# Kernel optimization log

Hardware: AMD Instinct MI355X
Metric: run time of the kernel (lower is better)

The kernel has to match this reference:

```python
import jax, jax.numpy as jnp
import numpy as np

H = 16
D_MODEL = 1024
D_K = D_MODEL // H
WINDOW = 50
ROPE_BASE = 10000.0


def _rope_tables(seq_len, dim, dtype):
    inv_freq = 1.0 / (ROPE_BASE ** (jnp.arange(0, dim, 2, dtype=jnp.float32) / dim))
    t = jnp.arange(seq_len, dtype=jnp.float32)
    freqs = t[:, None] * inv_freq[None, :]          # [S, dim/2]
    emb = jnp.concatenate([freqs, freqs], axis=-1)  # [S, dim]
    return jnp.cos(emb).astype(dtype), jnp.sin(emb).astype(dtype)


def _rotate_half(x):
    d = x.shape[-1] // 2
    return jnp.concatenate([-x[..., d:], x[..., :d]], axis=-1)


def setup_inputs() -> dict:
    key = jax.random.key(0)
    ks = jax.random.split(key, 11)
    B, S = 2, 2048
    scale = 1.0 / np.sqrt(D_MODEL)
    inp = {
        'query': jax.random.normal(ks[0], (B, S, D_MODEL), jnp.float32),
        'key':   jax.random.normal(ks[1], (B, S, D_MODEL), jnp.float32),
        'value': jax.random.normal(ks[2], (B, S, D_MODEL), jnp.float32),
        'Wq': jax.random.normal(ks[3], (D_MODEL, D_MODEL), jnp.float32) * scale,
        'bq': jnp.zeros((D_MODEL,), jnp.float32),
        'Wk': jax.random.normal(ks[4], (D_MODEL, D_MODEL), jnp.float32) * scale,
        'bk': jnp.zeros((D_MODEL,), jnp.float32),
        'Wv': jax.random.normal(ks[5], (D_MODEL, D_MODEL), jnp.float32) * scale,
        'bv': jnp.zeros((D_MODEL,), jnp.float32),
        'Wo': jax.random.normal(ks[6], (D_MODEL, D_MODEL), jnp.float32) * scale,
        'bo': jnp.zeros((D_MODEL,), jnp.float32),
    }
    return inp


def reference(query, key, value, Wq, bq, Wk, bk, Wv, bv, Wo, bo):
    B, S, _ = query.shape
    # QKV projections (torch Linear: x @ W.T + b), split into heads -> [B,H,S,Dk]
    def proj(x, W, b):
        return (x @ W.T + b).reshape(B, S, H, D_K).transpose(0, 2, 1, 3)
    q = proj(query, Wq, bq)
    k = proj(key, Wk, bk)
    v = proj(value, Wv, bv)

    cos, sin = _rope_tables(S, D_K, q.dtype)  # [S, Dk]
    q = q * cos + _rotate_half(q) * sin
    k = k * cos + _rotate_half(k) * sin

    scores = jnp.einsum('bhqd,bhkd->bhqk', q, k) / np.sqrt(D_K)
    # sliding-window mask: |i-j| <= WINDOW
    idx = jnp.arange(S)
    dist = jnp.abs(idx[None, :] - idx[:, None])  # [S, S]
    scores = jnp.where(dist <= WINDOW, scores, jnp.asarray(-1e9, scores.dtype))

    p = jax.nn.softmax(scores, axis=-1)
    out = jnp.einsum('bhqk,bhkd->bhqd', p, v)          # [B,H,S,Dk]
    out = out.transpose(0, 2, 1, 3).reshape(B, S, D_MODEL)
    return out @ Wo.T + bo
```

## Files before the change

kernel.cpp:

```cpp
#include <hip/hip_runtime.h>
#include <hip/hip_bf16.h>
#include <math.h>

typedef __bf16 bf16_t;
typedef __bf16 bf16x8 __attribute__((ext_vector_type(8)));
typedef float floatx4 __attribute__((ext_vector_type(4)));
typedef unsigned int u32;

#define NHEAD 16

__device__ __forceinline__ void gload_lds16(const void* g, void* l) {
    __builtin_amdgcn_global_load_lds((const __attribute__((address_space(1))) u32*)g,
                                     (__attribute__((address_space(3))) u32*)l, 16, 0, 0);
}

__global__ __launch_bounds__(256) void k_prep(
    const float* __restrict__ q, const float* __restrict__ k, const float* __restrict__ v,
    const float* __restrict__ wq, const float* __restrict__ wk,
    const float* __restrict__ wv, const float* __restrict__ wo,
    bf16_t* __restrict__ Xq, bf16_t* __restrict__ Xk, bf16_t* __restrict__ Xv,
    bf16_t* __restrict__ Wqb, bf16_t* __restrict__ Wkb, bf16_t* __restrict__ Wvb,
    bf16_t* __restrict__ Wob, float* __restrict__ ct, float* __restrict__ st)
{
    int b = blockIdx.x;
    if (b < 8192) {
        const float* src; bf16_t* dst; int off;
        if      (b < 2048) { src = q;  dst = Xq;  off = b; }
        else if (b < 4096) { src = k;  dst = Xk;  off = b - 2048; }
        else if (b < 6144) { src = v;  dst = Xv;  off = b - 4096; }
        else if (b < 6656) { src = wq; dst = Wqb; off = b - 6144; }
        else if (b < 7168) { src = wk; dst = Wkb; off = b - 6656; }
        else if (b < 7680) { src = wv; dst = Wvb; off = b - 7168; }
        else               { src = wo; dst = Wob; off = b - 7680; }
        int i = (off * 256 + threadIdx.x) * 8;
        float4 a = *(const float4*)(src + i);
        float4 c = *(const float4*)(src + i + 4);
        bf16x8 o;
        o[0]=(bf16_t)a.x; o[1]=(bf16_t)a.y; o[2]=(bf16_t)a.z; o[3]=(bf16_t)a.w;
        o[4]=(bf16_t)c.x; o[5]=(bf16_t)c.y; o[6]=(bf16_t)c.z; o[7]=(bf16_t)c.w;
        *(bf16x8*)(dst + i) = o;
    } else {
        int idx = (b - 8192) * 256 + threadIdx.x;
        int s = idx >> 5, i = idx & 31;
        float e = (float)(2 * i) / 64.0f;
        float invf = 1.0f / powf(10000.0f, e);
        float ang = (float)s * invf;
        ct[idx] = cosf(ang);
        st[idx] = sinf(ang);
    }
}

__global__ __launch_bounds__(256,2) void k_gemm_qkv(
    const bf16_t* __restrict__ Xq, const bf16_t* __restrict__ Xk, const bf16_t* __restrict__ Xv,
    const bf16_t* __restrict__ Wqb, const bf16_t* __restrict__ Wkb, const bf16_t* __restrict__ Wvb,
    const float* __restrict__ bq, const float* __restrict__ bk, const float* __restrict__ bv,
    bf16_t* __restrict__ Qr, bf16_t* __restrict__ Kr, bf16_t* __restrict__ Vh,
    const float* __restrict__ ct, const float* __restrict__ st)
{
    __shared__ bf16_t As[2][128*32];
    __shared__ bf16_t Bs[2][128*32];

    int b0 = blockIdx.x;
    int wg = (b0 & 7) * 96 + (b0 >> 3);
    int id  = wg >> 8;
    int bid = wg & 255;

    const bf16_t* A   = (id==0) ? Xq  : (id==1) ? Xk  : Xv;
    const bf16_t* Wt  = (id==0) ? Wqb : (id==1) ? Wkb : Wvb;
    const float*  bias= (id==0) ? bq  : (id==1) ? bk  : bv;
    bf16_t* out = (id==0) ? Qr : (id==1) ? Kr : Vh;
    bool do_rope = (id < 2);

    int bm = (bid >> 3) << 7;
    int bn = (bid & 7) << 7;
    int tid = threadIdx.x;
    int l = tid & 63, wid = tid >> 6;
    int wr = wid >> 1, wc = wid & 1;
    int lane16 = l & 15, hi8 = (l >> 4) << 3;

    floatx4 acc[4][4];
    #pragma unroll
    for (int i = 0; i < 4; ++i)
        #pragma unroll
        for (int j = 0; j < 4; ++j) acc[i][j] = (floatx4){0.f,0.f,0.f,0.f};

    int srow = tid >> 2, scol = (tid & 3) << 3;
    const bf16_t* Ab = A  + ((size_t)(bm + srow) << 10) + scol;
    const bf16_t* Bb = Wt + ((size_t)(bn + srow) << 10) + scol;

    #pragma unroll
    for (int i2 = 0; i2 < 2; ++i2) {
        gload_lds16(Ab + (i2 << 16), &As[0][(tid + (i2<<8)) << 3]);
        gload_lds16(Bb + (i2 << 16), &Bs[0][(tid + (i2<<8)) << 3]);
    }
    __syncthreads();

    int cur = 0;
    for (int t = 0; t < 32; ++t) {
        if (t < 31) {
            int k0 = (t + 1) << 5;
            #pragma unroll
            for (int i2 = 0; i2 < 2; ++i2) {
                gload_lds16(Ab + k0 + (i2 << 16), &As[cur^1][(tid + (i2<<8)) << 3]);
                gload_lds16(Bb + k0 + (i2 << 16), &Bs[cur^1][(tid + (i2<<8)) << 3]);
            }
        }
        bf16x8 af[4], bfr[4];
        #pragma unroll
        for (int i = 0; i < 4; ++i)
            af[i]  = *(const bf16x8*)&As[cur][((wr<<6) + (i<<4) + lane16)*32 + hi8];
        #pragma unroll
        for (int j = 0; j < 4; ++j)
            bfr[j] = *(const bf16x8*)&Bs[cur][((wc<<6) + (j<<4) + lane16)*32 + hi8];
        #pragma unroll
        for (int i = 0; i < 4; ++i)
            #pragma unroll
            for (int j = 0; j < 4; ++j)
                acc[i][j] = __builtin_amdgcn_mfma_f32_16x16x32_bf16(af[i], bfr[j], acc[i][j], 0, 0, 0);
        __syncthreads();
        cur ^= 1;
    }

    int h = (bn + (wc<<6)) >> 6;
    #pragma unroll
    for (int i = 0; i < 4; ++i) {
        #pragma unroll
        for (int r = 0; r < 4; ++r) {
            int m  = bm + (wr<<6) + (i<<4) + ((l>>4)<<2) + r;
            int b_ = m >> 11, s_ = m & 2047;
            size_t ob = ((((size_t)(b_*NHEAD + h)) << 11) + s_) << 6;
            if (do_rope) {
                #pragma unroll
                for (int j = 0; j < 2; ++j) {
                    int d = (j<<4) + lane16;
                    float lo = acc[i][j][r]   + bias[bn + (wc<<6) + d];
                    float hv = acc[i][j+2][r] + bias[bn + (wc<<6) + d + 32];
                    float c = ct[(s_<<5) + d], sn = st[(s_<<5) + d];
                    out[ob + d]      = (bf16_t)(lo*c - hv*sn);
                    out[ob + d + 32] = (bf16_t)(hv*c + lo*sn);
                }
            } else {
                #pragma unroll
                for (int j = 0; j < 4; ++j) {
                    int d = (j<<4) + lane16;
                    out[ob + d] = (bf16_t)(acc[i][j][r] + bias[bn + (wc<<6) + d]);
                }
            }
        }
    }
}

__global__ __launch_bounds__(256,2) void k_gemm_o(
    const bf16_t* __restrict__ A, const bf16_t* __restrict__ Wt,
    const float* __restrict__ bias, float* __restrict__ out)
{
    __shared__ bf16_t As[2][128*32];
    __shared__ bf16_t Bs[2][128*32];

    int b0 = blockIdx.x;
    int bid = (b0 & 7) * 32 + (b0 >> 3);
    int bm = (bid >> 3) << 7;
    int bn = (bid & 7) << 7;
    int tid = threadIdx.x;
    int l = tid & 63, wid = tid >> 6;
    int wr = wid >> 1, wc = wid & 1;
    int lane16 = l & 15, hi8 = (l >> 4) << 3;

    floatx4 acc[4][4];
    #pragma unroll
    for (int i = 0; i < 4; ++i)
        #pragma unroll
        for (int j = 0; j < 4; ++j) acc[i][j] = (floatx4){0.f,0.f,0.f,0.f};

    int srow = tid >> 2, scol = (tid & 3) << 3;
    const bf16_t* Ab = A  + ((size_t)(bm + srow) << 10) + scol;
    const bf16_t* Bb = Wt + ((size_t)(bn + srow) << 10) + scol;

    #pragma unroll
    for (int i2 = 0; i2 < 2; ++i2) {
        gload_lds16(Ab + (i2 << 16), &As[0][(tid + (i2<<8)) << 3]);
        gload_lds16(Bb + (i2 << 16), &Bs[0][(tid + (i2<<8)) << 3]);
    }
    __syncthreads();

    int cur = 0;
    for (int t = 0; t < 32; ++t) {
        if (t < 31) {
            int k0 = (t + 1) << 5;
            #pragma unroll
            for (int i2 = 0; i2 < 2; ++i2) {
                gload_lds16(Ab + k0 + (i2 << 16), &As[cur^1][(tid + (i2<<8)) << 3]);
                gload_lds16(Bb + k0 + (i2 << 16), &Bs[cur^1][(tid + (i2<<8)) << 3]);
            }
        }
        bf16x8 af[4], bfr[4];
        #pragma unroll
        for (int i = 0; i < 4; ++i)
            af[i]  = *(const bf16x8*)&As[cur][((wr<<6) + (i<<4) + lane16)*32 + hi8];
        #pragma unroll
        for (int j = 0; j < 4; ++j)
            bfr[j] = *(const bf16x8*)&Bs[cur][((wc<<6) + (j<<4) + lane16)*32 + hi8];
        #pragma unroll
        for (int i = 0; i < 4; ++i)
            #pragma unroll
            for (int j = 0; j < 4; ++j)
                acc[i][j] = __builtin_amdgcn_mfma_f32_16x16x32_bf16(af[i], bfr[j], acc[i][j], 0, 0, 0);
        __syncthreads();
        cur ^= 1;
    }

    #pragma unroll
    for (int i = 0; i < 4; ++i)
        #pragma unroll
        for (int r = 0; r < 4; ++r) {
            int m = bm + (wr<<6) + (i<<4) + ((l>>4)<<2) + r;
            #pragma unroll
            for (int j = 0; j < 4; ++j) {
                int n = bn + (wc<<6) + (j<<4) + lane16;
                out[((size_t)m << 10) + n] = acc[i][j][r] + bias[n];
            }
        }
}

__global__ __launch_bounds__(256,2) void k_attn(
    const bf16_t* __restrict__ Qr, const bf16_t* __restrict__ Kr,
    const bf16_t* __restrict__ Vh, bf16_t* __restrict__ AO)
{
    __shared__ char smem[51200];
    bf16_t* KsPs = (bf16_t*)smem;
    bf16_t* Vt   = (bf16_t*)(smem + 25600);

    int q0 = blockIdx.x << 6;
    int h = blockIdx.y, b_ = blockIdx.z;
    int kstart = q0 - 64; if (kstart < 0) kstart = 0;
    int kend   = q0 + 128; if (kend > 2048) kend = 2048;
    int NR = kend - kstart;

    int tid = threadIdx.x, l = tid & 63, w = tid >> 6;
    int lane16 = l & 15, hi8 = (l >> 4) << 3;

    const bf16_t* Kbase = Kr + (((((size_t)(b_*NHEAD + h)) << 11) + kstart) << 6);
    const bf16_t* Vbase = Vh + (((((size_t)(b_*NHEAD + h)) << 11) + kstart) << 6);

    #pragma unroll
    for (int it = 0; it < 6; ++it) {
        int c = tid + (it << 8);
        int y = c << 4;
        int row = y >> 7, oz = y & 127;
        int srw = row < NR ? row : NR - 1;
        int src = (srw << 7) + (oz ^ ((row & 7) << 4));
        gload_lds16((const char*)Kbase + src, (char*)KsPs + y);
    }
    #pragma unroll
    for (int it = 0; it < 6; ++it) {
        int c = tid + (it << 8);
        int jd = c >> 3, d0 = (c & 7) << 3;
        int js = jd < NR ? jd : NR - 1;
        bf16x8 v8 = *(const bf16x8*)(Vbase + (js << 6) + d0);
        #pragma unroll
        for (int t = 0; t < 8; ++t) Vt[(d0 + t) * 200 + jd] = v8[t];
    }
    int qs = q0 + (w << 4) + lane16;
    const bf16_t* Qbase = Qr + (((((size_t)(b_*NHEAD + h)) << 11) + qs) << 6);
    bf16x8 qf0 = *(const bf16x8*)(Qbase + hi8);
    bf16x8 qf1 = *(const bf16x8*)(Qbase + 32 + hi8);

    __syncthreads();

    floatx4 sc[12];
    #pragma unroll
    for (int kt = 0; kt < 12; ++kt) {
        int row = (kt << 4) + lane16;
        int base = (row << 7) + (hi8 << 1);
        int swz = (row & 7) << 4;
        bf16x8 kf0 = *(const bf16x8*)((const char*)KsPs + (base ^ swz));
        bf16x8 kf1 = *(const bf16x8*)((const char*)KsPs + ((base + 64) ^ swz));
        floatx4 a = (floatx4){0.f,0.f,0.f,0.f};
        a = __builtin_amdgcn_mfma_f32_16x16x32_bf16(qf0, kf0, a, 0, 0, 0);
        a = __builtin_amdgcn_mfma_f32_16x16x32_bf16(qf1, kf1, a, 0, 0, 0);
        sc[kt] = a;
    }

    float inv_[4];
    #pragma unroll
    for (int r = 0; r < 4; ++r) {
        int qrow = q0 + (w << 4) + ((l >> 4) << 2) + r;
        float mx = -1e30f;
        #pragma unroll
        for (int kt = 0; kt < 12; ++kt) {
            int ks = kstart + (kt << 4) + lane16;
            int dd = qrow - ks; dd = dd < 0 ? -dd : dd;
            float sv = sc[kt][r] * 0.125f;
            sv = (dd <= 50 && ks < kend) ? sv : -1e30f;
            sc[kt][r] = sv;
            mx = fmaxf(mx, sv);
        }
        #pragma unroll
        for (int off = 1; off < 16; off <<= 1) mx = fmaxf(mx, __shfl_xor(mx, off));
        float sum = 0.f;
        #pragma unroll
        for (int kt = 0; kt < 12; ++kt) {
            float p = __expf(sc[kt][r] - mx);
            sc[kt][r] = p;
            sum += p;
        }
        #pragma unroll
        for (int off = 1; off < 16; off <<= 1) sum += __shfl_xor(sum, off);
        inv_[r] = 1.0f / sum;
    }

    __syncthreads();

    bf16_t* Pw = KsPs + w * 16 * 200;
    #pragma unroll
    for (int r = 0; r < 4; ++r) {
        int prow = ((l >> 4) << 2) + r;
        #pragma unroll
        for (int kt = 0; kt < 12; ++kt)
            Pw[prow * 200 + (kt << 4) + lane16] = (bf16_t)(sc[kt][r] * inv_[r]);
    }

    floatx4 oc[4];
    #pragma unroll
    for (int dt = 0; dt < 4; ++dt) oc[dt] = (floatx4){0.f,0.f,0.f,0.f};
    #pragma unroll
    for (int ks = 0; ks < 6; ++ks) {
        bf16x8 pf = *(const bf16x8*)&Pw[lane16 * 200 + (ks << 5) + hi8];
        #pragma unroll
        for (int dt = 0; dt < 4; ++dt) {
            bf16x8 vf = *(const bf16x8*)&Vt[((dt << 4) + lane16) * 200 + (ks << 5) + hi8];
            oc[dt] = __builtin_amdgcn_mfma_f32_16x16x32_bf16(pf, vf, oc[dt], 0, 0, 0);
        }
    }
    #pragma unroll
    for (int dt = 0; dt < 4; ++dt)
        #pragma unroll
        for (int r = 0; r < 4; ++r) {
            int qq = q0 + (w << 4) + ((l >> 4) << 2) + r;
            AO[(((size_t)(b_ * 2048 + qq)) << 10) + (h << 6) + (dt << 4) + lane16] = (bf16_t)oc[dt][r];
        }
}

extern "C" void kernel_launch(void* const* d_in, const int* in_sizes, int n_in,
                              void* d_out, int out_size, void* d_ws, size_t ws_size,
                              hipStream_t stream)
{
    const float* query = (const float*)d_in[0];
    const float* key_  = (const float*)d_in[1];
    const float* value = (const float*)d_in[2];
    const float* Wq = (const float*)d_in[3];
    const float* bq = (const float*)d_in[4];
    const float* Wk = (const float*)d_in[5];
    const float* bk = (const float*)d_in[6];
    const float* Wv = (const float*)d_in[7];
    const float* bv = (const float*)d_in[8];
    const float* Wo = (const float*)d_in[9];
    const float* bo = (const float*)d_in[10];

    char* ws = (char*)d_ws;
    bf16_t* Xq  = (bf16_t*)(ws);
    bf16_t* Xk  = (bf16_t*)(ws + 8388608);
    bf16_t* Xv  = (bf16_t*)(ws + 16777216);
    bf16_t* Wqb = (bf16_t*)(ws + 25165824);
    bf16_t* Wkb = (bf16_t*)(ws + 27262976);
    bf16_t* Wvb = (bf16_t*)(ws + 29360128);
    bf16_t* Wob = (bf16_t*)(ws + 31457280);
    bf16_t* Qr  = (bf16_t*)(ws + 33554432);
    bf16_t* Kr  = (bf16_t*)(ws + 41943040);
    bf16_t* Vh  = (bf16_t*)(ws + 50331648);
    bf16_t* AO  = (bf16_t*)(ws + 58720256);
    float*  ct  = (float*)(ws + 67108864);
    float*  st  = (float*)(ws + 67371008);

    k_prep<<<8448, 256, 0, stream>>>(query, key_, value, Wq, Wk, Wv, Wo,
                                     Xq, Xk, Xv, Wqb, Wkb, Wvb, Wob, ct, st);
    k_gemm_qkv<<<768, 256, 0, stream>>>(Xq, Xk, Xv, Wqb, Wkb, Wvb,
                                        bq, bk, bv, Qr, Kr, Vh, ct, st);
    k_attn<<<dim3(32, 16, 2), 256, 0, stream>>>(Qr, Kr, Vh, AO);
    k_gemm_o<<<256, 256, 0, stream>>>(AO, Wob, bo, (float*)d_out);
}
```

Measured before the change: 97.61 us.

## Rewrite QKV GEMM with 256x256 tiles, 512 threads, swizzled LDS and interleaved staging

The QKV projection GEMM moves from 128x128 tiles with 256 threads and BK=32 to 256x256 tiles with 512 threads (8 waves) and BK=64, double-buffered in 128KB of LDS with an XOR swizzle. Global-to-LDS staging for the next K tile is spread across the MFMA phases, with explicit barriers, waitcnt and setprio. This is meant to raise operand reuse per LDS load, cut bank conflicts and hide load latency. The cost is fewer workgroups (192 on a large CU count), heavy LDS use that limits occupancy to one block per CU, and higher register pressure from 32 accumulators per thread.

```diff
diff --git a/kernel.cpp b/kernel.cpp
--- a/kernel.cpp
+++ b/kernel.cpp
@@ -12,6 +12,14 @@
 __device__ __forceinline__ void gload_lds16(const void* g, void* l) {
     __builtin_amdgcn_global_load_lds((const __attribute__((address_space(1))) u32*)g,
                                      (__attribute__((address_space(3))) u32*)l, 16, 0, 0);
+}
+
+__device__ __forceinline__ void bar() {
+    __builtin_amdgcn_sched_barrier(0);
+    asm volatile("" ::: "memory");
+    __builtin_amdgcn_s_barrier();
+    asm volatile("" ::: "memory");
+    __builtin_amdgcn_sched_barrier(0);
 }
 
 __global__ __launch_bounds__(256) void k_prep(
@@ -50,20 +58,29 @@
     }
 }
 
-__global__ __launch_bounds__(256,2) void k_gemm_qkv(
+#define STAGE_TILE(Gbase, rowoff, tt, Ldst) do {                                   \
+    _Pragma("unroll")                                                              \
+    for (int it_ = 0; it_ < 4; ++it_) {                                            \
+        int row_ = (it_ << 6) + srow;                                              \
+        const char* s_ = (const char*)(Gbase) + (((size_t)((rowoff) + row_)) << 11)\
+                         + ((tt) << 7) + scol;                                     \
+        gload_lds16(s_, (Ldst) + (it_ << 13) + (tid << 4));                        \
+    }                                                                              \
+} while (0)
+
+__global__ __launch_bounds__(512, 2) void k_gemm_qkv(
     const bf16_t* __restrict__ Xq, const bf16_t* __restrict__ Xk, const bf16_t* __restrict__ Xv,
     const bf16_t* __restrict__ Wqb, const bf16_t* __restrict__ Wkb, const bf16_t* __restrict__ Wvb,
     const float* __restrict__ bq, const float* __restrict__ bk, const float* __restrict__ bv,
     bf16_t* __restrict__ Qr, bf16_t* __restrict__ Kr, bf16_t* __restrict__ Vh,
     const float* __restrict__ ct, const float* __restrict__ st)
 {
-    __shared__ bf16_t As[2][128*32];
-    __shared__ bf16_t Bs[2][128*32];
+    __shared__ __align__(16) char smem[131072];
 
     int b0 = blockIdx.x;
-    int wg = (b0 & 7) * 96 + (b0 >> 3);
-    int id  = wg >> 8;
-    int bid = wg & 255;
+    int wg = (b0 & 7) * 24 + (b0 >> 3);
+    int id  = wg >> 6;
+    int bid = wg & 63;
 
     const bf16_t* A   = (id==0) ? Xq  : (id==1) ? Xk  : Xv;
     const bf16_t* Wt  = (id==0) ? Wqb : (id==1) ? Wkb : Wvb;
@@ -71,79 +88,103 @@
     bf16_t* out = (id==0) ? Qr : (id==1) ? Kr : Vh;
     bool do_rope = (id < 2);
 
-    int bm = (bid >> 3) << 7;
-    int bn = (bid & 7) << 7;
+    int bm = (bid >> 2) << 8;
+    int bn = (bid & 3) << 8;
     int tid = threadIdx.x;
     int l = tid & 63, wid = tid >> 6;
-    int wr = wid >> 1, wc = wid & 1;
-    int lane16 = l & 15, hi8 = (l >> 4) << 3;
-
-    floatx4 acc[4][4];
-    #pragma unroll
-    for (int i = 0; i < 4; ++i)
+    int wr = wid >> 2, wc = wid & 3;
+    int lane16 = l & 15;
+    int hi16 = (l >> 4) << 4;
+    int swz = (lane16 & 7) << 4;
+    int arow_base = ((wr << 7) + lane16) << 7;
+    int brow_base = ((wc << 6) + lane16) << 7;
+
+    int srow = tid >> 3;
+    int scol = ((tid & 7) << 4) ^ ((srow & 7) << 4);
+
+    floatx4 acc[8][4];
+    #pragma unroll
+    for (int i = 0; i < 8; ++i)
         #pragma unroll
         for (int j = 0; j < 4; ++j) acc[i][j] = (floatx4){0.f,0.f,0.f,0.f};
 
-    int srow = tid >> 2, scol = (tid & 3) << 3;
-    const bf16_t* Ab = A  + ((size_t)(bm + srow) << 10) + scol;
-    const bf16_t* Bb = Wt + ((size_t)(bn + srow) << 10) + scol;
-
-    #pragma unroll
-    for (int i2 = 0; i2 < 2; ++i2) {
-        gload_lds16(Ab + (i2 << 16), &As[0][(tid + (i2<<8)) << 3]);
-        gload_lds16(Bb + (i2 << 16), &Bs[0][(tid + (i2<<8)) << 3]);
-    }
-    __syncthreads();
-
-    int cur = 0;
-    for (int t = 0; t < 32; ++t) {
-        if (t < 31) {
-            int k0 = (t + 1) << 5;
+    STAGE_TILE(A,  bm, 0, smem);
+    STAGE_TILE(Wt, bn, 0, smem + 32768);
+    STAGE_TILE(A,  bm, 1, smem + 65536);
+    STAGE_TILE(Wt, bn, 1, smem + 65536 + 32768);
+    asm volatile("s_waitcnt vmcnt(8)" ::: "memory");
+    bar();
+
+    bf16x8 bfrag[4][2];
+    for (int t = 0; t < 16; ++t) {
+        int c = t & 1;
+        char* Ac = smem + (c << 16);
+        char* Bc = Ac + 32768;
+        char* An = smem + ((c ^ 1) << 16);
+        char* Bn = An + 32768;
+        bool do_stage = (t >= 1) && (t < 15);
+
+        #pragma unroll
+        for (int p = 0; p < 4; ++p) {
+            bf16x8 af[2][2];
             #pragma unroll
-            for (int i2 = 0; i2 < 2; ++i2) {
-                gload_lds16(Ab + k0 + (i2 << 16), &As[cur^1][(tid + (i2<<8)) << 3]);
-                gload_lds16(Bb + k0 + (i2 << 16), &Bs[cur^1][(tid + (i2<<8)) << 3]);
+            for (int ip = 0; ip < 2; ++ip)
+                #pragma unroll
+                for (int s = 0; s < 2; ++s)
+                    af[ip][s] = *(const bf16x8*)(Ac + arow_base + (((p<<1)+ip) << 11)
+                                                 + (((s<<6) + hi16) ^ swz));
+            if (p == 0) {
+                #pragma unroll
+                for (int j = 0; j < 4; ++j)
+                    #pragma unroll
+                    for (int s = 0; s < 2; ++s)
+                        bfrag[j][s] = *(const bf16x8*)(Bc + brow_base + (j << 11)
+                                                       + (((s<<6) + hi16) ^ swz));
+                if (do_stage) STAGE_TILE(A, bm, t + 1, An);
+            } else if (p == 1) {
+                if (do_stage) STAGE_TILE(Wt, bn, t + 1, Bn);
             }
-        }
-        bf16x8 af[4], bfr[4];
-        #pragma unroll
-        for (int i = 0; i < 4; ++i)
-            af[i]  = *(const bf16x8*)&As[cur][((wr<<6) + (i<<4) + lane16)*32 + hi8];
-        #pragma unroll
-        for (int j = 0; j < 4; ++j)
-            bfr[j] = *(const bf16x8*)&Bs[cur][((wc<<6) + (j<<4) + lane16)*32 + hi8];
-        #pragma unroll
-        for (int i = 0; i < 4; ++i)
+            bar();
+            __builtin_amdgcn_s_setprio(1);
             #pragma unroll
-            for (int j = 0; j < 4; ++j)
-                acc[i][j] = __builtin_amdgcn_mfma_f32_16x16x32_bf16(af[i], bfr[j], acc[i][j], 0, 0, 0);
-        __syncthreads();
-        cur ^= 1;
-    }
-
-    int h = (bn + (wc<<6)) >> 6;
-    #pragma unroll
-    for (int i = 0; i < 4; ++i) {
+            for (int ip = 0; ip < 2; ++ip)
+                #pragma unroll
+                for (int j = 0; j < 4; ++j) {
+                    floatx4 tmp = __builtin_amdgcn_mfma_f32_16x16x32_bf16(
+                                      af[ip][0], bfrag[j][0], acc[(p<<1)+ip][j], 0, 0, 0);
+                    acc[(p<<1)+ip][j] = __builtin_amdgcn_mfma_f32_16x16x32_bf16(
+                                      af[ip][1], bfrag[j][1], tmp, 0, 0, 0);
+                }
+            __builtin_amdgcn_s_setprio(0);
+            if (p == 3) asm volatile("s_waitcnt vmcnt(0)" ::: "memory");
+            bar();
+        }
+    }
+
+    int h = (bn >> 6) + wc;
+    int nb = bn + (wc << 6);
+    #pragma unroll
+    for (int i = 0; i < 8; ++i) {
         #pragma unroll
         for (int r = 0; r < 4; ++r) {
-            int m  = bm + (wr<<6) + (i<<4) + ((l>>4)<<2) + r;
+            int m  = bm + (wr << 7) + (i << 4) + ((l >> 4) << 2) + r;
             int b_ = m >> 11, s_ = m & 2047;
-            size_t ob = ((((size_t)(b_*NHEAD + h)) << 11) + s_) << 6;
+            size_t ob = ((((size_t)(b_ * NHEAD + h)) << 11) + s_) << 6;
             if (do_rope) {
                 #pragma unroll
                 for (int j = 0; j < 2; ++j) {
-                    int d = (j<<4) + lane16;
-                    float lo = acc[i][j][r]   + bias[bn + (wc<<6) + d];
-                    float hv = acc[i][j+2][r] + bias[bn + (wc<<6) + d + 32];
-                    float c = ct[(s_<<5) + d], sn = st[(s_<<5) + d];
-                    out[ob + d]      = (bf16_t)(lo*c - hv*sn);
-                    out[ob + d + 32] = (bf16_t)(hv*c + lo*sn);
+                    int d = (j << 4) + lane16;
+                    float lo = acc[i][j][r]     + bias[nb + d];
+                    float hv = acc[i][j + 2][r] + bias[nb + d + 32];
+                    float cc = ct[(s_ << 5) + d], sn = st[(s_ << 5) + d];
+                    out[ob + d]      = (bf16_t)(lo * cc - hv * sn);
+                    out[ob + d + 32] = (bf16_t)(hv * cc + lo * sn);
                 }
             } else {
                 #pragma unroll
                 for (int j = 0; j < 4; ++j) {
-                    int d = (j<<4) + lane16;
-                    out[ob + d] = (bf16_t)(acc[i][j][r] + bias[bn + (wc<<6) + d]);
+                    int d = (j << 4) + lane16;
+                    out[ob + d] = (bf16_t)(acc[i][j][r] + bias[nb + d]);
                 }
             }
         }
@@ -374,7 +415,7 @@
 
     k_prep<<<8448, 256, 0, stream>>>(query, key_, value, Wq, Wk, Wv, Wo,
                                      Xq, Xk, Xv, Wqb, Wkb, Wvb, Wob, ct, st);
-    k_gemm_qkv<<<768, 256, 0, stream>>>(Xq, Xk, Xv, Wqb, Wkb, Wvb,
+    k_gemm_qkv<<<192, 512, 0, stream>>>(Xq, Xk, Xv, Wqb, Wkb, Wvb,
                                         bq, bk, bv, Qr, Kr, Vh, ct, st);
     k_attn<<<dim3(32, 16, 2), 256, 0, stream>>>(Qr, Kr, Vh, AO);
     k_gemm_o<<<256, 256, 0, stream>>>(AO, Wob, bo, (float*)d_out);
```

New measurement: 101.8 us. 4.3% more time.

## Fuse fp32 activation conversion into QKV GEMM and triple-buffer both GEMMs

Applied to the files above, without the earlier changes.

The QKV GEMM now reads the fp32 query/key/value directly, converting to bf16 in registers and writing them to LDS, so the prep kernel no longer makes a bf16 copy of the activations. This removes a full read and write pass over the three activation tensors. Both GEMMs switch from double to triple-buffered LDS with a prefetch distance of two, using explicit waitcnt and fenced barriers, and occupancy hints are raised to 3. The tradeoff is more LDS per block, twice the A-tile global traffic inside the GEMM (fp32 instead of bf16), and register pressure from holding staged values across the MFMA block.

```diff
diff --git a/kernel.cpp b/kernel.cpp
--- a/kernel.cpp
+++ b/kernel.cpp
@@ -14,33 +14,38 @@
                                      (__attribute__((address_space(3))) u32*)l, 16, 0, 0);
 }
 
+__device__ __forceinline__ void write8(bf16_t* p, float4 a, float4 b) {
+    bf16x8 o;
+    o[0]=(bf16_t)a.x; o[1]=(bf16_t)a.y; o[2]=(bf16_t)a.z; o[3]=(bf16_t)a.w;
+    o[4]=(bf16_t)b.x; o[5]=(bf16_t)b.y; o[6]=(bf16_t)b.z; o[7]=(bf16_t)b.w;
+    *(bf16x8*)p = o;
+}
+
+__device__ __forceinline__ void bar_fenced() {
+    __builtin_amdgcn_sched_barrier(0);
+    __builtin_amdgcn_s_barrier();
+    __builtin_amdgcn_sched_barrier(0);
+}
+
 __global__ __launch_bounds__(256) void k_prep(
-    const float* __restrict__ q, const float* __restrict__ k, const float* __restrict__ v,
     const float* __restrict__ wq, const float* __restrict__ wk,
     const float* __restrict__ wv, const float* __restrict__ wo,
-    bf16_t* __restrict__ Xq, bf16_t* __restrict__ Xk, bf16_t* __restrict__ Xv,
     bf16_t* __restrict__ Wqb, bf16_t* __restrict__ Wkb, bf16_t* __restrict__ Wvb,
     bf16_t* __restrict__ Wob, float* __restrict__ ct, float* __restrict__ st)
 {
     int b = blockIdx.x;
-    if (b < 8192) {
+    if (b < 2048) {
         const float* src; bf16_t* dst; int off;
-        if      (b < 2048) { src = q;  dst = Xq;  off = b; }
-        else if (b < 4096) { src = k;  dst = Xk;  off = b - 2048; }
-        else if (b < 6144) { src = v;  dst = Xv;  off = b - 4096; }
-        else if (b < 6656) { src = wq; dst = Wqb; off = b - 6144; }
-        else if (b < 7168) { src = wk; dst = Wkb; off = b - 6656; }
-        else if (b < 7680) { src = wv; dst = Wvb; off = b - 7168; }
-        else               { src = wo; dst = Wob; off = b - 7680; }
+        if      (b < 512)  { src = wq; dst = Wqb; off = b; }
+        else if (b < 1024) { src = wk; dst = Wkb; off = b - 512; }
+        else if (b < 1536) { src = wv; dst = Wvb; off = b - 1024; }
+        else               { src = wo; dst = Wob; off = b - 1536; }
         int i = (off * 256 + threadIdx.x) * 8;
         float4 a = *(const float4*)(src + i);
         float4 c = *(const float4*)(src + i + 4);
-        bf16x8 o;
-        o[0]=(bf16_t)a.x; o[1]=(bf16_t)a.y; o[2]=(bf16_t)a.z; o[3]=(bf16_t)a.w;
-        o[4]=(bf16_t)c.x; o[5]=(bf16_t)c.y; o[6]=(bf16_t)c.z; o[7]=(bf16_t)c.w;
-        *(bf16x8*)(dst + i) = o;
+        write8(dst + i, a, c);
     } else {
-        int idx = (b - 8192) * 256 + threadIdx.x;
+        int idx = (b - 2048) * 256 + threadIdx.x;
         int s = idx >> 5, i = idx & 31;
         float e = (float)(2 * i) / 64.0f;
         float invf = 1.0f / powf(10000.0f, e);
@@ -50,22 +55,22 @@
     }
 }
 
-__global__ __launch_bounds__(256,2) void k_gemm_qkv(
-    const bf16_t* __restrict__ Xq, const bf16_t* __restrict__ Xk, const bf16_t* __restrict__ Xv,
+__global__ __launch_bounds__(256,3) void k_gemm_qkv(
+    const float* __restrict__ Xq, const float* __restrict__ Xk, const float* __restrict__ Xv,
     const bf16_t* __restrict__ Wqb, const bf16_t* __restrict__ Wkb, const bf16_t* __restrict__ Wvb,
     const float* __restrict__ bq, const float* __restrict__ bk, const float* __restrict__ bv,
     bf16_t* __restrict__ Qr, bf16_t* __restrict__ Kr, bf16_t* __restrict__ Vh,
     const float* __restrict__ ct, const float* __restrict__ st)
 {
-    __shared__ bf16_t As[2][128*32];
-    __shared__ bf16_t Bs[2][128*32];
+    __shared__ __align__(16) bf16_t As[3][4096];
+    __shared__ __align__(16) bf16_t Bs[3][4096];
 
     int b0 = blockIdx.x;
     int wg = (b0 & 7) * 96 + (b0 >> 3);
     int id  = wg >> 8;
     int bid = wg & 255;
 
-    const bf16_t* A   = (id==0) ? Xq  : (id==1) ? Xk  : Xv;
+    const float*  A   = (id==0) ? Xq  : (id==1) ? Xk  : Xv;
     const bf16_t* Wt  = (id==0) ? Wqb : (id==1) ? Wkb : Wvb;
     const float*  bias= (id==0) ? bq  : (id==1) ? bk  : bv;
     bf16_t* out = (id==0) ? Qr : (id==1) ? Kr : Vh;
@@ -84,41 +89,70 @@
         #pragma unroll
         for (int j = 0; j < 4; ++j) acc[i][j] = (floatx4){0.f,0.f,0.f,0.f};
 
-    int srow = tid >> 2, scol = (tid & 3) << 3;
-    const bf16_t* Ab = A  + ((size_t)(bm + srow) << 10) + scol;
-    const bf16_t* Bb = Wt + ((size_t)(bn + srow) << 10) + scol;
-
-    #pragma unroll
-    for (int i2 = 0; i2 < 2; ++i2) {
-        gload_lds16(Ab + (i2 << 16), &As[0][(tid + (i2<<8)) << 3]);
-        gload_lds16(Bb + (i2 << 16), &Bs[0][(tid + (i2<<8)) << 3]);
-    }
-    __syncthreads();
-
-    int cur = 0;
+    int c0 = tid, c1 = tid + 256;
+    int row0 = c0 >> 2, col0 = (c0 & 3) << 3;
+    int row1 = c1 >> 2, col1 = (c1 & 3) << 3;
+    const float*  Ap0 = A  + ((size_t)(bm + row0) << 10) + col0;
+    const float*  Ap1 = A  + ((size_t)(bm + row1) << 10) + col1;
+    const bf16_t* Bp0 = Wt + ((size_t)(bn + row0) << 10) + col0;
+    const bf16_t* Bp1 = Wt + ((size_t)(bn + row1) << 10) + col1;
+
+    {
+        float4 p0 = *(const float4*)(Ap0);      float4 p1 = *(const float4*)(Ap0 + 4);
+        float4 p2 = *(const float4*)(Ap1);      float4 p3 = *(const float4*)(Ap1 + 4);
+        gload_lds16(Bp0, &Bs[0][c0 << 3]);
+        gload_lds16(Bp1, &Bs[0][c1 << 3]);
+        float4 q0 = *(const float4*)(Ap0 + 32); float4 q1 = *(const float4*)(Ap0 + 36);
+        float4 q2 = *(const float4*)(Ap1 + 32); float4 q3 = *(const float4*)(Ap1 + 36);
+        gload_lds16(Bp0 + 32, &Bs[1][c0 << 3]);
+        gload_lds16(Bp1 + 32, &Bs[1][c1 << 3]);
+        write8(&As[0][c0 << 3], p0, p1);  write8(&As[0][c1 << 3], p2, p3);
+        write8(&As[1][c0 << 3], q0, q1);  write8(&As[1][c1 << 3], q2, q3);
+        asm volatile("s_waitcnt vmcnt(0) lgkmcnt(0)" ::: "memory");
+        bar_fenced();
+    }
+
+    int cur = 0, nxt2 = 2;
     for (int t = 0; t < 32; ++t) {
-        if (t < 31) {
-            int k0 = (t + 1) << 5;
-            #pragma unroll
-            for (int i2 = 0; i2 < 2; ++i2) {
-                gload_lds16(Ab + k0 + (i2 << 16), &As[cur^1][(tid + (i2<<8)) << 3]);
-                gload_lds16(Bb + k0 + (i2 << 16), &Bs[cur^1][(tid + (i2<<8)) << 3]);
-            }
-        }
+        const bf16_t* Ac = As[cur];
+        const bf16_t* Bc = Bs[cur];
+        bf16_t* Ast = As[nxt2];
+        bf16_t* Bst = Bs[nxt2];
+        bool stg = (t < 30);
+
+        float4 p0, p1, p2, p3;
+        if (stg) {
+            int k0 = (t + 2) << 5;
+            p0 = *(const float4*)(Ap0 + k0);      p1 = *(const float4*)(Ap0 + k0 + 4);
+            p2 = *(const float4*)(Ap1 + k0);      p3 = *(const float4*)(Ap1 + k0 + 4);
+            gload_lds16(Bp0 + k0, &Bst[c0 << 3]);
+            gload_lds16(Bp1 + k0, &Bst[c1 << 3]);
+        }
+
         bf16x8 af[4], bfr[4];
         #pragma unroll
         for (int i = 0; i < 4; ++i)
-            af[i]  = *(const bf16x8*)&As[cur][((wr<<6) + (i<<4) + lane16)*32 + hi8];
+            af[i]  = *(const bf16x8*)&Ac[((wr<<6) + (i<<4) + lane16)*32 + hi8];
         #pragma unroll
         for (int j = 0; j < 4; ++j)
-            bfr[j] = *(const bf16x8*)&Bs[cur][((wc<<6) + (j<<4) + lane16)*32 + hi8];
+            bfr[j] = *(const bf16x8*)&Bc[((wc<<6) + (j<<4) + lane16)*32 + hi8];
         #pragma unroll
         for (int i = 0; i < 4; ++i)
             #pragma unroll
             for (int j = 0; j < 4; ++j)
                 acc[i][j] = __builtin_amdgcn_mfma_f32_16x16x32_bf16(af[i], bfr[j], acc[i][j], 0, 0, 0);
-        __syncthreads();
-        cur ^= 1;
+
+        if (stg) {
+            write8(&Ast[c0 << 3], p0, p1);
+            write8(&Ast[c1 << 3], p2, p3);
+        }
+        if (t < 31) {
+            if (!stg) asm volatile("s_waitcnt vmcnt(0)" ::: "memory");
+            asm volatile("s_waitcnt lgkmcnt(0)" ::: "memory");
+            bar_fenced();
+        }
+        cur  = (cur  == 2) ? 0 : cur + 1;
+        nxt2 = (nxt2 == 2) ? 0 : nxt2 + 1;
     }
 
     int h = (bn + (wc<<6)) >> 6;
@@ -150,12 +184,12 @@
     }
 }
 
-__global__ __launch_bounds__(256,2) void k_gemm_o(
+__global__ __launch_bounds__(256,3) void k_gemm_o(
     const bf16_t* __restrict__ A, const bf16_t* __restrict__ Wt,
     const float* __restrict__ bias, float* __restrict__ out)
 {
-    __shared__ bf16_t As[2][128*32];
-    __shared__ bf16_t Bs[2][128*32];
+    __shared__ __align__(16) bf16_t As[3][4096];
+    __shared__ __align__(16) bf16_t Bs[3][4096];
 
     int b0 = blockIdx.x;
     int bid = (b0 & 7) * 32 + (b0 >> 3);
@@ -172,41 +206,55 @@
         #pragma unroll
         for (int j = 0; j < 4; ++j) acc[i][j] = (floatx4){0.f,0.f,0.f,0.f};
 
-    int srow = tid >> 2, scol = (tid & 3) << 3;
-    const bf16_t* Ab = A  + ((size_t)(bm + srow) << 10) + scol;
-    const bf16_t* Bb = Wt + ((size_t)(bn + srow) << 10) + scol;
-
-    #pragma unroll
-    for (int i2 = 0; i2 < 2; ++i2) {
-        gload_lds16(Ab + (i2 << 16), &As[0][(tid + (i2<<8)) << 3]);
-        gload_lds16(Bb + (i2 << 16), &Bs[0][(tid + (i2<<8)) << 3]);
-    }
-    __syncthreads();
-
-    int cur = 0;
+    int c0 = tid, c1 = tid + 256;
+    int row0 = c0 >> 2, col0 = (c0 & 3) << 3;
+    int row1 = c1 >> 2, col1 = (c1 & 3) << 3;
+    const bf16_t* Ap0 = A  + ((size_t)(bm + row0) << 10) + col0;
+    const bf16_t* Ap1 = A  + ((size_t)(bm + row1) << 10) + col1;
+    const bf16_t* Bp0 = Wt + ((size_t)(bn + row0) << 10) + col0;
+    const bf16_t* Bp1 = Wt + ((size_t)(bn + row1) << 10) + col1;
+
+    gload_lds16(Ap0, &As[0][c0 << 3]);  gload_lds16(Ap1, &As[0][c1 << 3]);
+    gload_lds16(Bp0, &Bs[0][c0 << 3]);  gload_lds16(Bp1, &Bs[0][c1 << 3]);
+    gload_lds16(Ap0 + 32, &As[1][c0 << 3]);  gload_lds16(Ap1 + 32, &As[1][c1 << 3]);
+    gload_lds16(Bp0 + 32, &Bs[1][c0 << 3]);  gload_lds16(Bp1 + 32, &Bs[1][c1 << 3]);
+    asm volatile("s_waitcnt vmcnt(4)" ::: "memory");
+    bar_fenced();
+
+    int cur = 0, nxt2 = 2;
     for (int t = 0; t < 32; ++t) {
-        if (t < 31) {
-            int k0 = (t + 1) << 5;
-            #pragma unroll
-            for (int i2 = 0; i2 < 2; ++i2) {
-                gload_lds16(Ab + k0 + (i2 << 16), &As[cur^1][(tid + (i2<<8)) << 3]);
-                gload_lds16(Bb + k0 + (i2 << 16), &Bs[cur^1][(tid + (i2<<8)) << 3]);
-            }
-        }
+        const bf16_t* Ac = As[cur];
+        const bf16_t* Bc = Bs[cur];
+        bf16_t* Ast = As[nxt2];
+        bf16_t* Bst = Bs[nxt2];
+        bool stg = (t < 30);
+
+        if (stg) {
+            int k0 = (t + 2) << 5;
+            gload_lds16(Ap0 + k0, &Ast[c0 << 3]);  gload_lds16(Ap1 + k0, &Ast[c1 << 3]);
+            gload_lds16(Bp0 + k0, &Bst[c0 << 3]);  gload_lds16(Bp1 + k0, &Bst[c1 << 3]);
+        }
+
         bf16x8 af[4], bfr[4];
         #pragma unroll
         for (int i = 0; i < 4; ++i)
-            af[i]  = *(const bf16x8*)&As[cur][((wr<<6) + (i<<4) + lane16)*32 + hi8];
+            af[i]  = *(const bf16x8*)&Ac[((wr<<6) + (i<<4) + lane16)*32 + hi8];
         #pragma unroll
         for (int j = 0; j < 4; ++j)
-            bfr[j] = *(const bf16x8*)&Bs[cur][((wc<<6) + (j<<4) + lane16)*32 + hi8];
+            bfr[j] = *(const bf16x8*)&Bc[((wc<<6) + (j<<4) + lane16)*32 + hi8];
         #pragma unroll
         for (int i = 0; i < 4; ++i)
             #pragma unroll
             for (int j = 0; j < 4; ++j)
                 acc[i][j] = __builtin_amdgcn_mfma_f32_16x16x32_bf16(af[i], bfr[j], acc[i][j], 0, 0, 0);
-        __syncthreads();
-        cur ^= 1;
+
+        if (t < 31) {
+            if (stg) asm volatile("s_waitcnt vmcnt(4)" ::: "memory");
+            else     asm volatile("s_waitcnt vmcnt(0)" ::: "memory");
+            bar_fenced();
+        }
+        cur  = (cur  == 2) ? 0 : cur + 1;
+        nxt2 = (nxt2 == 2) ? 0 : nxt2 + 1;
     }
 
     #pragma unroll
@@ -358,23 +406,19 @@
     const float* bo = (const float*)d_in[10];
 
     char* ws = (char*)d_ws;
-    bf16_t* Xq  = (bf16_t*)(ws);
-    bf16_t* Xk  = (bf16_t*)(ws + 8388608);
-    bf16_t* Xv  = (bf16_t*)(ws + 16777216);
-    bf16_t* Wqb = (bf16_t*)(ws + 25165824);
-    bf16_t* Wkb = (bf16_t*)(ws + 27262976);
-    bf16_t* Wvb = (bf16_t*)(ws + 29360128);
-    bf16_t* Wob = (bf16_t*)(ws + 31457280);
-    bf16_t* Qr  = (bf16_t*)(ws + 33554432);
-    bf16_t* Kr  = (bf16_t*)(ws + 41943040);
-    bf16_t* Vh  = (bf16_t*)(ws + 50331648);
-    bf16_t* AO  = (bf16_t*)(ws + 58720256);
-    float*  ct  = (float*)(ws + 67108864);
-    float*  st  = (float*)(ws + 67371008);
-
-    k_prep<<<8448, 256, 0, stream>>>(query, key_, value, Wq, Wk, Wv, Wo,
-                                     Xq, Xk, Xv, Wqb, Wkb, Wvb, Wob, ct, st);
-    k_gemm_qkv<<<768, 256, 0, stream>>>(Xq, Xk, Xv, Wqb, Wkb, Wvb,
+    bf16_t* Wqb = (bf16_t*)(ws);
+    bf16_t* Wkb = (bf16_t*)(ws + 2097152);
+    bf16_t* Wvb = (bf16_t*)(ws + 4194304);
+    bf16_t* Wob = (bf16_t*)(ws + 6291456);
+    bf16_t* Qr  = (bf16_t*)(ws + 8388608);
+    bf16_t* Kr  = (bf16_t*)(ws + 16777216);
+    bf16_t* Vh  = (bf16_t*)(ws + 25165824);
+    bf16_t* AO  = (bf16_t*)(ws + 33554432);
+    float*  ct  = (float*)(ws + 41943040);
+    float*  st  = (float*)(ws + 42205184);
+
+    k_prep<<<2304, 256, 0, stream>>>(Wq, Wk, Wv, Wo, Wqb, Wkb, Wvb, Wob, ct, st);
+    k_gemm_qkv<<<768, 256, 0, stream>>>(query, key_, value, Wqb, Wkb, Wvb,
                                         bq, bk, bv, Qr, Kr, Vh, ct, st);
     k_attn<<<dim3(32, 16, 2), 256, 0, stream>>>(Qr, Kr, Vh, AO);
     k_gemm_o<<<256, 256, 0, stream>>>(AO, Wob, bo, (float*)d_out);
```

Result: slower. 100.8 us (+3.3%).

## Triple-buffer GEMM LDS tiles with prefetch depth two and fragment-ordered layout

Applied to the files above, without the earlier changes.

Both projection GEMMs move from double to triple LDS buffering, so loads run two K-steps ahead. Explicit vmcnt waits plus sched-barrier-fenced s_barrier replace __syncthreads, letting only the older loads be waited on. The LDS tile is re-laid out in MFMA fragment order (16-row by 32-col chunks) so each lane's 16-byte read is contiguous, which should avoid bank conflicts. Launch bounds go to 3 blocks per SM; the larger LDS footprint (48KB) and register pressure may limit occupancy, and the hand-written waitcnt logic is fragile.

```diff
diff --git a/kernel.cpp b/kernel.cpp
--- a/kernel.cpp
+++ b/kernel.cpp
@@ -12,6 +12,12 @@
 __device__ __forceinline__ void gload_lds16(const void* g, void* l) {
     __builtin_amdgcn_global_load_lds((const __attribute__((address_space(1))) u32*)g,
                                      (__attribute__((address_space(3))) u32*)l, 16, 0, 0);
+}
+
+__device__ __forceinline__ void bar_fenced() {
+    __builtin_amdgcn_sched_barrier(0);
+    __builtin_amdgcn_s_barrier();
+    __builtin_amdgcn_sched_barrier(0);
 }
 
 __global__ __launch_bounds__(256) void k_prep(
@@ -50,15 +56,16 @@
     }
 }
 
-__global__ __launch_bounds__(256,2) void k_gemm_qkv(
+
+__global__ __launch_bounds__(256,3) void k_gemm_qkv(
     const bf16_t* __restrict__ Xq, const bf16_t* __restrict__ Xk, const bf16_t* __restrict__ Xv,
     const bf16_t* __restrict__ Wqb, const bf16_t* __restrict__ Wkb, const bf16_t* __restrict__ Wvb,
     const float* __restrict__ bq, const float* __restrict__ bk, const float* __restrict__ bv,
     bf16_t* __restrict__ Qr, bf16_t* __restrict__ Kr, bf16_t* __restrict__ Vh,
     const float* __restrict__ ct, const float* __restrict__ st)
 {
-    __shared__ bf16_t As[2][128*32];
-    __shared__ bf16_t Bs[2][128*32];
+    __shared__ __align__(16) bf16_t As[3][4096];
+    __shared__ __align__(16) bf16_t Bs[3][4096];
 
     int b0 = blockIdx.x;
     int wg = (b0 & 7) * 96 + (b0 >> 3);
@@ -76,7 +83,7 @@
     int tid = threadIdx.x;
     int l = tid & 63, wid = tid >> 6;
     int wr = wid >> 1, wc = wid & 1;
-    int lane16 = l & 15, hi8 = (l >> 4) << 3;
+    int lane16 = l & 15;
 
     floatx4 acc[4][4];
     #pragma unroll
@@ -84,41 +91,51 @@
         #pragma unroll
         for (int j = 0; j < 4; ++j) acc[i][j] = (floatx4){0.f,0.f,0.f,0.f};
 
-    int srow = tid >> 2, scol = (tid & 3) << 3;
-    const bf16_t* Ab = A  + ((size_t)(bm + srow) << 10) + scol;
-    const bf16_t* Bb = Wt + ((size_t)(bn + srow) << 10) + scol;
-
-    #pragma unroll
-    for (int i2 = 0; i2 < 2; ++i2) {
-        gload_lds16(Ab + (i2 << 16), &As[0][(tid + (i2<<8)) << 3]);
-        gload_lds16(Bb + (i2 << 16), &Bs[0][(tid + (i2<<8)) << 3]);
-    }
-    __syncthreads();
-
-    int cur = 0;
+    int c0 = tid, c1 = tid + 256;
+    int row0 = ((c0 >> 6) << 4) + (c0 & 15), sl0 = ((c0 >> 4) & 3) << 3;
+    int row1 = ((c1 >> 6) << 4) + (c1 & 15), sl1 = ((c1 >> 4) & 3) << 3;
+    const bf16_t* Ap0 = A  + ((size_t)(bm + row0) << 10) + sl0;
+    const bf16_t* Ap1 = A  + ((size_t)(bm + row1) << 10) + sl1;
+    const bf16_t* Bp0 = Wt + ((size_t)(bn + row0) << 10) + sl0;
+    const bf16_t* Bp1 = Wt + ((size_t)(bn + row1) << 10) + sl1;
+
+    gload_lds16(Ap0, &As[0][c0 << 3]);       gload_lds16(Ap1, &As[0][c1 << 3]);
+    gload_lds16(Bp0, &Bs[0][c0 << 3]);       gload_lds16(Bp1, &Bs[0][c1 << 3]);
+    gload_lds16(Ap0 + 32, &As[1][c0 << 3]);  gload_lds16(Ap1 + 32, &As[1][c1 << 3]);
+    gload_lds16(Bp0 + 32, &Bs[1][c0 << 3]);  gload_lds16(Bp1 + 32, &Bs[1][c1 << 3]);
+    asm volatile("s_waitcnt vmcnt(4)" ::: "memory");
+    bar_fenced();
+
+    int a_off = ((l >> 4) << 8) + (lane16 << 4);
+    int cur = 0, nxt2 = 2;
     for (int t = 0; t < 32; ++t) {
-        if (t < 31) {
-            int k0 = (t + 1) << 5;
-            #pragma unroll
-            for (int i2 = 0; i2 < 2; ++i2) {
-                gload_lds16(Ab + k0 + (i2 << 16), &As[cur^1][(tid + (i2<<8)) << 3]);
-                gload_lds16(Bb + k0 + (i2 << 16), &Bs[cur^1][(tid + (i2<<8)) << 3]);
-            }
+        bool stg = (t < 30);
+        if (stg) {
+            int k0 = (t + 2) << 5;
+            gload_lds16(Ap0 + k0, &As[nxt2][c0 << 3]);
+            gload_lds16(Ap1 + k0, &As[nxt2][c1 << 3]);
+            gload_lds16(Bp0 + k0, &Bs[nxt2][c0 << 3]);
+            gload_lds16(Bp1 + k0, &Bs[nxt2][c1 << 3]);
         }
         bf16x8 af[4], bfr[4];
         #pragma unroll
         for (int i = 0; i < 4; ++i)
-            af[i]  = *(const bf16x8*)&As[cur][((wr<<6) + (i<<4) + lane16)*32 + hi8];
+            af[i]  = *(const bf16x8*)((const char*)As[cur] + ((((wr << 2) + i)) << 10) + a_off);
         #pragma unroll
         for (int j = 0; j < 4; ++j)
-            bfr[j] = *(const bf16x8*)&Bs[cur][((wc<<6) + (j<<4) + lane16)*32 + hi8];
+            bfr[j] = *(const bf16x8*)((const char*)Bs[cur] + ((((wc << 2) + j)) << 10) + a_off);
         #pragma unroll
         for (int i = 0; i < 4; ++i)
             #pragma unroll
             for (int j = 0; j < 4; ++j)
                 acc[i][j] = __builtin_amdgcn_mfma_f32_16x16x32_bf16(af[i], bfr[j], acc[i][j], 0, 0, 0);
-        __syncthreads();
-        cur ^= 1;
+        if (t < 31) {
+            if (stg) asm volatile("s_waitcnt vmcnt(4)" ::: "memory");
+            else     asm volatile("s_waitcnt vmcnt(0)" ::: "memory");
+            bar_fenced();
+        }
+        cur  = (cur  == 2) ? 0 : cur + 1;
+        nxt2 = (nxt2 == 2) ? 0 : nxt2 + 1;
     }
 
     int h = (bn + (wc<<6)) >> 6;
@@ -150,12 +167,12 @@
     }
 }
 
-__global__ __launch_bounds__(256,2) void k_gemm_o(
+__global__ __launch_bounds__(256,3) void k_gemm_o(
     const bf16_t* __restrict__ A, const bf16_t* __restrict__ Wt,
     const float* __restrict__ bias, float* __restrict__ out)
 {
-    __shared__ bf16_t As[2][128*32];
-    __shared__ bf16_t Bs[2][128*32];
+    __shared__ __align__(16) bf16_t As[3][4096];
+    __shared__ __align__(16) bf16_t Bs[3][4096];
 
     int b0 = blockIdx.x;
     int bid = (b0 & 7) * 32 + (b0 >> 3);
@@ -164,7 +181,7 @@
     int tid = threadIdx.x;
     int l = tid & 63, wid = tid >> 6;
     int wr = wid >> 1, wc = wid & 1;
-    int lane16 = l & 15, hi8 = (l >> 4) << 3;
+    int lane16 = l & 15;
 
     floatx4 acc[4][4];
     #pragma unroll
@@ -172,41 +189,51 @@
         #pragma unroll
         for (int j = 0; j < 4; ++j) acc[i][j] = (floatx4){0.f,0.f,0.f,0.f};
 
-    int srow = tid >> 2, scol = (tid & 3) << 3;
-    const bf16_t* Ab = A  + ((size_t)(bm + srow) << 10) + scol;
-    const bf16_t* Bb = Wt + ((size_t)(bn + srow) << 10) + scol;
-
-    #pragma unroll
-    for (int i2 = 0; i2 < 2; ++i2) {
-        gload_lds16(Ab + (i2 << 16), &As[0][(tid + (i2<<8)) << 3]);
-        gload_lds16(Bb + (i2 << 16), &Bs[0][(tid + (i2<<8)) << 3]);
-    }
-    __syncthreads();
-
-    int cur = 0;
+    int c0 = tid, c1 = tid + 256;
+    int row0 = ((c0 >> 6) << 4) + (c0 & 15), sl0 = ((c0 >> 4) & 3) << 3;
+    int row1 = ((c1 >> 6) << 4) + (c1 & 15), sl1 = ((c1 >> 4) & 3) << 3;
+    const bf16_t* Ap0 = A  + ((size_t)(bm + row0) << 10) + sl0;
+    const bf16_t* Ap1 = A  + ((size_t)(bm + row1) << 10) + sl1;
+    const bf16_t* Bp0 = Wt + ((size_t)(bn + row0) << 10) + sl0;
+    const bf16_t* Bp1 = Wt + ((size_t)(bn + row1) << 10) + sl1;
+
+    gload_lds16(Ap0, &As[0][c0 << 3]);       gload_lds16(Ap1, &As[0][c1 << 3]);
+    gload_lds16(Bp0, &Bs[0][c0 << 3]);       gload_lds16(Bp1, &Bs[0][c1 << 3]);
+    gload_lds16(Ap0 + 32, &As[1][c0 << 3]);  gload_lds16(Ap1 + 32, &As[1][c1 << 3]);
+    gload_lds16(Bp0 + 32, &Bs[1][c0 << 3]);  gload_lds16(Bp1 + 32, &Bs[1][c1 << 3]);
+    asm volatile("s_waitcnt vmcnt(4)" ::: "memory");
+    bar_fenced();
+
+    int a_off = ((l >> 4) << 8) + (lane16 << 4);
+    int cur = 0, nxt2 = 2;
     for (int t = 0; t < 32; ++t) {
-        if (t < 31) {
-            int k0 = (t + 1) << 5;
-            #pragma unroll
-            for (int i2 = 0; i2 < 2; ++i2) {
-                gload_lds16(Ab + k0 + (i2 << 16), &As[cur^1][(tid + (i2<<8)) << 3]);
-                gload_lds16(Bb + k0 + (i2 << 16), &Bs[cur^1][(tid + (i2<<8)) << 3]);
-            }
+        bool stg = (t < 30);
+        if (stg) {
+            int k0 = (t + 2) << 5;
+            gload_lds16(Ap0 + k0, &As[nxt2][c0 << 3]);
+            gload_lds16(Ap1 + k0, &As[nxt2][c1 << 3]);
+            gload_lds16(Bp0 + k0, &Bs[nxt2][c0 << 3]);
+            gload_lds16(Bp1 + k0, &Bs[nxt2][c1 << 3]);
         }
         bf16x8 af[4], bfr[4];
         #pragma unroll
         for (int i = 0; i < 4; ++i)
-            af[i]  = *(const bf16x8*)&As[cur][((wr<<6) + (i<<4) + lane16)*32 + hi8];
+            af[i]  = *(const bf16x8*)((const char*)As[cur] + ((((wr << 2) + i)) << 10) + a_off);
         #pragma unroll
         for (int j = 0; j < 4; ++j)
-            bfr[j] = *(const bf16x8*)&Bs[cur][((wc<<6) + (j<<4) + lane16)*32 + hi8];
+            bfr[j] = *(const bf16x8*)((const char*)Bs[cur] + ((((wc << 2) + j)) << 10) + a_off);
         #pragma unroll
         for (int i = 0; i < 4; ++i)
             #pragma unroll
             for (int j = 0; j < 4; ++j)
                 acc[i][j] = __builtin_amdgcn_mfma_f32_16x16x32_bf16(af[i], bfr[j], acc[i][j], 0, 0, 0);
-        __syncthreads();
-        cur ^= 1;
+        if (t < 31) {
+            if (stg) asm volatile("s_waitcnt vmcnt(4)" ::: "memory");
+            else     asm volatile("s_waitcnt vmcnt(0)" ::: "memory");
+            bar_fenced();
+        }
+        cur  = (cur  == 2) ? 0 : cur + 1;
+        nxt2 = (nxt2 == 2) ? 0 : nxt2 + 1;
     }
 
     #pragma unroll
```

Result: slower. 122.8 us (+25.8%).
